# Kernel tuning notes

Hardware: AMD Instinct MI355X
Metric: run time of the kernel (lower is better)

The kernel has to match this reference:

```python
import jax, jax.numpy as jnp
import numpy as np

D_MODEL = 1024
NUM_HEADS = 16
HEAD_DIM = D_MODEL // NUM_HEADS
MAX_SEQ_LEN = 1024
BATCH = 2
SEQ = 1024


def setup_inputs() -> dict:
    key = jax.random.key(0)
    ks = jax.random.split(key, 12)
    s = 1.0 / np.sqrt(D_MODEL)
    inp = {
        "q": jax.random.normal(ks[0], (BATCH, SEQ, D_MODEL), jnp.float32),
        "k": jax.random.normal(ks[1], (BATCH, SEQ, D_MODEL), jnp.float32),
        "v": jax.random.normal(ks[2], (BATCH, SEQ, D_MODEL), jnp.float32),
        # causal mask (broadcast over batch and heads); masked_fill where mask==0
        "mask": jnp.tril(jnp.ones((SEQ, SEQ), jnp.bool_))[None, None, :, :],
        "Wq": jax.random.normal(ks[3], (D_MODEL, D_MODEL), jnp.float32) * s,
        "bq": jnp.zeros((D_MODEL,), jnp.float32),
        "Wk": jax.random.normal(ks[4], (D_MODEL, D_MODEL), jnp.float32) * s,
        "bk": jnp.zeros((D_MODEL,), jnp.float32),
        "Wv": jax.random.normal(ks[5], (D_MODEL, D_MODEL), jnp.float32) * s,
        "bv": jnp.zeros((D_MODEL,), jnp.float32),
        "Wo": jax.random.normal(ks[6], (D_MODEL, D_MODEL), jnp.float32) * s,
        "bo": jnp.zeros((D_MODEL,), jnp.float32),
        # relative-position embedding table (requires_grad=False in original)
        "e_r": jax.random.normal(ks[7], (MAX_SEQ_LEN, HEAD_DIM), jnp.float32),
    }
    return inp


def _skew(qe):
    # qe: (b, h, q, L) -> pad last dim on the left, reshape, drop first row
    b, h, q, L = qe.shape
    s = jnp.pad(qe, ((0, 0), (0, 0), (0, 0), (1, 0)))  # (b,h,q,L+1)
    s = s.reshape(b, h, L + 1, q)
    return s[:, :, 1:, :]  # (b,h,L,q)


def _rel_position_mask(q_len, L, dtype):
    # keep qe[i, j] where j >= L - 1 - i (upper-right skewed triangle)
    rows = jnp.arange(q_len)
    cols = jnp.arange(L)
    return (cols[None, :] >= (L - 1 - rows)[:, None]).astype(dtype)


def reference(q, k, v, mask, Wq, bq, Wk, bk, Wv, bv, Wo, bo, e_r):
    B, S, _ = q.shape
    def split_heads(x):
        return x.reshape(B, -1, NUM_HEADS, HEAD_DIM).transpose(0, 2, 1, 3)

    qh = split_heads(q @ Wq + bq)  # (B,H,S,D)
    kh = split_heads(k @ Wk + bk)
    vh = split_heads(v @ Wv + bv)

    q_len = qh.shape[2]
    e_sub = e_r[max(0, MAX_SEQ_LEN - q_len):, :]  # (L, D), L = min(q_len, MAX)
    qe = jnp.einsum('bhqd,kd->bhqk', qh, e_sub)  # (B,H,q,L)
    pm = _rel_position_mask(q_len, e_sub.shape[0], qe.dtype)
    qe = qe * pm[None, None, :, :]
    S_rel = _skew(qe)  # (B,H,L,q) == (B,H,S,S)

    scores = jnp.einsum('bhqd,bhkd->bhqk', qh, kh) / np.sqrt(HEAD_DIM)
    if mask is not None:
        scores = jnp.where(mask, scores, -1e9)
    attn = jax.nn.softmax(scores + S_rel, axis=-1)
    out = jnp.einsum('bhqk,bhkd->bhqd', attn, vh)
    out = out.transpose(0, 2, 1, 3).reshape(B, -1, D_MODEL)
    out = out @ Wo + bo
    return out, S_rel, qe
```

## Files before the change

### kernel.cpp

```cpp
#include <hip/hip_runtime.h>
#include <hip/hip_bf16.h>

typedef unsigned short u16;
typedef __attribute__((ext_vector_type(8))) short    bf16x8;
typedef __attribute__((ext_vector_type(8))) unsigned short u16x8;
typedef __attribute__((ext_vector_type(4))) float    f32x4;

#define SEQ    1024
#define DMODEL 1024
#define NHEAD  16
#define HDIM   64

#define OUT_OFF_SREL 2097152UL
#define OUT_OFF_QE   35651584UL

#define MFMA16(a, b, c) __builtin_amdgcn_mfma_f32_16x16x32_bf16((a), (b), (c), 0, 0, 0)

__device__ __forceinline__ float b2f(u16 u) {
    union { unsigned int i; float f; } x; x.i = ((unsigned int)u) << 16; return x.f;
}
__device__ __forceinline__ u16 f2b(float f) {
    union { __hip_bfloat16 h; u16 u; } x; x.h = __float2bfloat16(f); return x.u;
}
__device__ __forceinline__ void st_out(void* p, size_t idx, float v, int isf32) {
    if (isf32) ((float*)p)[idx] = v;
    else       ((u16*)p)[idx]   = f2b(v);
}

__global__ __launch_bounds__(256)
void k_detect(const u16* __restrict__ q, unsigned* __restrict__ flag)
{
    __shared__ int cnt;
    if (threadIdx.x == 0) cnt = 0;
    __syncthreads();
    int plaus = 0;
    for (int i = threadIdx.x; i < 4096; i += 256) {
        u16 u = q[2 * i];
        int e = (u >> 7) & 0xFF;
        if (e >= 102 && e <= 130) plaus++;
    }
    atomicAdd(&cnt, plaus);
    __syncthreads();
    if (threadIdx.x == 0) *flag = (cnt < 2048) ? 1u : 0u;
}

__global__ __launch_bounds__(256)
void k_conv(const void* __restrict__ src, u16* __restrict__ dst, int n4,
            const unsigned* __restrict__ flag)
{
    int i = blockIdx.x * 256 + threadIdx.x;
    if (i >= n4) return;
    if (*flag) {
        float4 f = ((const float4*)src)[i];
        ushort4 o;
        o.x = f2b(f.x); o.y = f2b(f.y); o.z = f2b(f.z); o.w = f2b(f.w);
        ((ushort4*)dst)[i] = o;
    } else {
        ((ushort4*)dst)[i] = ((const ushort4*)src)[i];
    }
}

__global__ __launch_bounds__(256)
void k_convT(const void* __restrict__ src, u16* __restrict__ dst,
             const unsigned* __restrict__ flag)
{
    __shared__ u16 tile[64][65];
    const int t  = threadIdx.x;
    const int n0 = blockIdx.x * 64;
    const int k0 = blockIdx.y * 64;
    const int isf32 = (*flag != 0u);

    #pragma unroll
    for (int i = 0; i < 4; ++i) {
        int idx = i * 256 + t;
        int r  = idx >> 4;
        int cg = (idx & 15) << 2;
        if (isf32) {
            float4 f = *(const float4*)((const float*)src + (size_t)(k0 + r) * 1024 + n0 + cg);
            tile[cg + 0][r] = f2b(f.x); tile[cg + 1][r] = f2b(f.y);
            tile[cg + 2][r] = f2b(f.z); tile[cg + 3][r] = f2b(f.w);
        } else {
            ushort4 u = *(const ushort4*)((const u16*)src + (size_t)(k0 + r) * 1024 + n0 + cg);
            tile[cg + 0][r] = u.x; tile[cg + 1][r] = u.y;
            tile[cg + 2][r] = u.z; tile[cg + 3][r] = u.w;
        }
    }
    __syncthreads();
    #pragma unroll
    for (int i = 0; i < 4; ++i) {
        int idx = i * 256 + t;
        int nl = idx >> 4;
        int kg = (idx & 15) << 2;
        ushort4 o;
        o.x = tile[nl][kg + 0]; o.y = tile[nl][kg + 1];
        o.z = tile[nl][kg + 2]; o.w = tile[nl][kg + 3];
        *(ushort4*)(dst + (size_t)(n0 + nl) * 1024 + k0 + kg) = o;
    }
}

__global__ __launch_bounds__(256)
void k_gemm(const u16* __restrict__ Aq, const u16* __restrict__ Ak, const u16* __restrict__ Av,
            const u16* __restrict__ Wtq, const u16* __restrict__ Wtk, const u16* __restrict__ Wtv,
            const u16* __restrict__ Bq, const u16* __restrict__ Bk, const u16* __restrict__ Bv,
            u16* __restrict__ Oq, u16* __restrict__ Ok, u16* __restrict__ Ov,
            void* __restrict__ out_flat, const unsigned* __restrict__ flag, int mode)
{
    __shared__ __align__(16) u16 Xs[128][72];
    __shared__ __align__(16) u16 Ws[128][72];

    const int z = blockIdx.z;
    const u16* A  = (z == 0) ? Aq : (z == 1) ? Ak : Av;
    const u16* Wt = (z == 0) ? Wtq : (z == 1) ? Wtk : Wtv;
    const u16* Bi = (z == 0) ? Bq : (z == 1) ? Bk : Bv;
    u16* O = (z == 0) ? Oq : (z == 1) ? Ok : Ov;

    const int t    = threadIdx.x;
    const int lane = t & 63;
    const int w    = t >> 6;
    const int q4   = lane >> 4;
    const int l16  = lane & 15;
    const int wy   = w >> 1, wx = w & 1;
    const int m0   = blockIdx.y * 128;
    const int n0   = blockIdx.x * 128;

    f32x4 acc[4][4] = {};

    for (int k0 = 0; k0 < DMODEL; k0 += 64) {
        __syncthreads();
        #pragma unroll
        for (int i = 0; i < 4; ++i) {
            int idx = i * 256 + t;
            int row = idx >> 3;
            int kg  = (idx & 7) << 3;
            *(u16x8*)&Xs[row][kg] = *(const u16x8*)(A  + (size_t)(m0 + row) * 1024 + k0 + kg);
            *(u16x8*)&Ws[row][kg] = *(const u16x8*)(Wt + (size_t)(n0 + row) * 1024 + k0 + kg);
        }
        __syncthreads();
        #pragma unroll
        for (int kc = 0; kc < 2; ++kc) {
            bf16x8 af[4], bfr[4];
            #pragma unroll
            for (int mt = 0; mt < 4; ++mt)
                af[mt] = *(const bf16x8*)&Xs[wy * 64 + mt * 16 + l16][kc * 32 + q4 * 8];
            #pragma unroll
            for (int nt = 0; nt < 4; ++nt)
                bfr[nt] = *(const bf16x8*)&Ws[wx * 64 + nt * 16 + l16][kc * 32 + q4 * 8];
            #pragma unroll
            for (int mt = 0; mt < 4; ++mt)
                #pragma unroll
                for (int nt = 0; nt < 4; ++nt)
                    acc[mt][nt] = MFMA16(af[mt], bfr[nt], acc[mt][nt]);
        }
    }

    const int isf32 = (*flag != 0u);
    float bias[4];
    #pragma unroll
    for (int nt = 0; nt < 4; ++nt) bias[nt] = b2f(Bi[n0 + wx * 64 + nt * 16 + l16]);

    #pragma unroll
    for (int mt = 0; mt < 4; ++mt) {
        #pragma unroll
        for (int nt = 0; nt < 4; ++nt) {
            #pragma unroll
            for (int reg = 0; reg < 4; ++reg) {
                const int m = m0 + wy * 64 + mt * 16 + q4 * 4 + reg;
                const int n = n0 + wx * 64 + nt * 16 + l16;
                const float v = acc[mt][nt][reg] + bias[nt];
                if (mode == 0) {
                    const int b = m >> 10, s = m & 1023, h = n >> 6, d = n & 63;
                    O[(((size_t)(b * NHEAD + h)) * SEQ + s) * HDIM + d] = f2b(v);
                } else {
                    st_out(out_flat, (size_t)m * DMODEL + n, v, isf32);
                }
            }
        }
    }
}

__global__ __launch_bounds__(256)
void k_qe(const u16* __restrict__ qh, const u16* __restrict__ er,
          void* __restrict__ out, const unsigned* __restrict__ flag)
{
    const int t    = threadIdx.x;
    const int lane = t & 63;
    const int w    = t >> 6;
    const int q4   = lane >> 4;
    const int l16  = lane & 15;
    const int bh   = blockIdx.x;
    const int r0   = blockIdx.y * 64;
    const int isf32 = (*flag != 0u);

    bf16x8 aQ[2];
    #pragma unroll
    for (int kc = 0; kc < 2; ++kc)
        aQ[kc] = *(const bf16x8*)(qh + ((size_t)bh * SEQ + r0 + w * 16 + l16) * HDIM + kc * 32 + q4 * 8);

    for (int jc = 0; jc < 16; ++jc) {
        f32x4 acc[4] = {};
        #pragma unroll
        for (int kc = 0; kc < 2; ++kc) {
            #pragma unroll
            for (int nt = 0; nt < 4; ++nt) {
                bf16x8 bfr = *(const bf16x8*)(er + (size_t)(jc * 64 + nt * 16 + l16) * HDIM + kc * 32 + q4 * 8);
                acc[nt] = MFMA16(aQ[kc], bfr, acc[nt]);
            }
        }
        #pragma unroll
        for (int nt = 0; nt < 4; ++nt) {
            #pragma unroll
            for (int reg = 0; reg < 4; ++reg) {
                const int r = r0 + w * 16 + q4 * 4 + reg;
                const int j = jc * 64 + nt * 16 + l16;
                const size_t base = (size_t)bh * (SEQ * SEQ) + (size_t)r * SEQ;
                const float v = acc[nt][reg];
                if (j + r >= SEQ - 1) {
                    st_out(out, OUT_OFF_QE   + base + j,                   v, isf32);
                    st_out(out, OUT_OFF_SREL + base + (j + r - (SEQ - 1)), v, isf32);
                } else {
                    st_out(out, OUT_OFF_QE   + base + j,           0.f, isf32);
                    st_out(out, OUT_OFF_SREL + base + (r + 1 + j), 0.f, isf32);
                }
            }
        }
    }
}

__global__ __launch_bounds__(256)
void k_attn(const u16* __restrict__ qh, const u16* __restrict__ kh, const u16* __restrict__ vh,
            const u16* __restrict__ er, u16* __restrict__ opre)
{
    __shared__ __align__(16) u16 Ks[64][72];
    __shared__ __align__(16) u16 Vt[64][72];
    __shared__ __align__(16) u16 Es[128][72];
    __shared__ float Rs[4][16][130];
    __shared__ __align__(16) u16 Ps[4][16][72];

    const int t    = threadIdx.x;
    const int lane = t & 63;
    const int w    = t >> 6;
    const int q4   = lane >> 4;
    const int l16  = lane & 15;
    const int bh   = blockIdx.x;
    const int qt   = 15 - blockIdx.y;
    const int r0   = qt * 64;

    bf16x8 aQ[2];
    #pragma unroll
    for (int kc = 0; kc < 2; ++kc)
        aQ[kc] = *(const bf16x8*)(qh + ((size_t)bh * SEQ + r0 + w * 16 + l16) * HDIM + kc * 32 + q4 * 8);

    f32x4 Oacc[4] = {};
    float mi[4] = { -1e30f, -1e30f, -1e30f, -1e30f };
    float li[4] = {};

    for (int tt = 0; tt <= qt; ++tt) {
        const int c0 = tt * 64;
        const int jbase = 960 + c0 - r0;
        const int diag = (tt == qt);

        __syncthreads();
        #pragma unroll
        for (int i = 0; i < 2; ++i) {
            int idx = i * 256 + t;
            int row = idx >> 3, kg = (idx & 7) << 3;
            *(u16x8*)&Ks[row][kg] = *(const u16x8*)(kh + ((size_t)bh * SEQ + c0 + row) * HDIM + kg);
        }
        #pragma unroll
        for (int i = 0; i < 4; ++i) {
            int idx = i * 256 + t;
            int c = idx >> 4, dg = (idx & 15) << 2;
            ushort4 v = *(const ushort4*)(vh + ((size_t)bh * SEQ + c0 + c) * HDIM + dg);
            Vt[dg + 0][c] = v.x; Vt[dg + 1][c] = v.y;
            Vt[dg + 2][c] = v.z; Vt[dg + 3][c] = v.w;
        }
        #pragma unroll
        for (int i = 0; i < 4; ++i) {
            int idx = i * 256 + t;
            int row = idx >> 3, kg = (idx & 7) << 3;
            int j = jbase + row; if (j > 1023) j = 1023;
            *(u16x8*)&Es[row][kg] = *(const u16x8*)(er + (size_t)j * HDIM + kg);
        }
        __syncthreads();

        {
            f32x4 Racc[8] = {};
            #pragma unroll
            for (int kc = 0; kc < 2; ++kc) {
                #pragma unroll
                for (int nt = 0; nt < 8; ++nt) {
                    bf16x8 bfr = *(const bf16x8*)&Es[nt * 16 + l16][kc * 32 + q4 * 8];
                    Racc[nt] = MFMA16(aQ[kc], bfr, Racc[nt]);
                }
            }
            #pragma unroll
            for (int nt = 0; nt < 8; ++nt)
                #pragma unroll
                for (int reg = 0; reg < 4; ++reg)
                    Rs[w][q4 * 4 + reg][nt * 16 + l16] = Racc[nt][reg];
        }

        f32x4 Sacc[4] = {};
        #pragma unroll
        for (int kc = 0; kc < 2; ++kc) {
            #pragma unroll
            for (int nt = 0; nt < 4; ++nt) {
                bf16x8 bfr = *(const bf16x8*)&Ks[nt * 16 + l16][kc * 32 + q4 * 8];
                Sacc[nt] = MFMA16(aQ[kc], bfr, Sacc[nt]);
            }
        }

        #pragma unroll
        for (int reg = 0; reg < 4; ++reg) {
            const int m16  = q4 * 4 + reg;
            const int mloc = w * 16 + m16;
            float sv[4];
            #pragma unroll
            for (int nt = 0; nt < 4; ++nt) {
                const int nloc = nt * 16 + l16;
                const int jj = 63 + nloc - mloc;
                float s = Sacc[nt][reg] * 0.125f + Rs[w][m16][jj];
                if (diag && (nloc > mloc)) s = -1e30f;
                sv[nt] = s;
            }
            float mx = fmaxf(fmaxf(sv[0], sv[1]), fmaxf(sv[2], sv[3]));
            #pragma unroll
            for (int off = 1; off < 16; off <<= 1) mx = fmaxf(mx, __shfl_xor(mx, off));
            const float mnew = fmaxf(mi[reg], mx);
            const float al   = __expf(mi[reg] - mnew);
            mi[reg] = mnew;
            float psum = 0.f;
            #pragma unroll
            for (int nt = 0; nt < 4; ++nt) {
                const float p = __expf(sv[nt] - mnew);
                psum += p;
                Ps[w][m16][nt * 16 + l16] = f2b(p);
            }
            #pragma unroll
            for (int off = 1; off < 16; off <<= 1) psum += __shfl_xor(psum, off);
            li[reg] = li[reg] * al + psum;
            #pragma unroll
            for (int dt = 0; dt < 4; ++dt) Oacc[dt][reg] *= al;
        }

        #pragma unroll
        for (int kc = 0; kc < 2; ++kc) {
            bf16x8 aP = *(const bf16x8*)&Ps[w][l16][kc * 32 + q4 * 8];
            #pragma unroll
            for (int dt = 0; dt < 4; ++dt) {
                bf16x8 bV = *(const bf16x8*)&Vt[dt * 16 + l16][kc * 32 + q4 * 8];
                Oacc[dt] = MFMA16(aP, bV, Oacc[dt]);
            }
        }
    }

    const int b = bh >> 4, h = bh & 15;
    #pragma unroll
    for (int dt = 0; dt < 4; ++dt) {
        #pragma unroll
        for (int reg = 0; reg < 4; ++reg) {
            const int r = r0 + w * 16 + q4 * 4 + reg;
            const int d = dt * 16 + l16;
            opre[((size_t)b * SEQ + r) * DMODEL + h * HDIM + d] = f2b(Oacc[dt][reg] / li[reg]);
        }
    }
}

extern "C" void kernel_launch(void* const* d_in, const int* in_sizes, int n_in,
                              void* d_out, int out_size, void* d_ws, size_t ws_size,
                              hipStream_t stream)
{
    u16* ws16 = (u16*)d_ws;
    unsigned* flag = (unsigned*)d_ws;
    u16* cq   = ws16 + 8;
    u16* ck   = cq   + 2097152;
    u16* cv   = ck   + 2097152;
    u16* cwqT = cv   + 2097152;
    u16* cwkT = cwqT + 1048576;
    u16* cwvT = cwkT + 1048576;
    u16* cwoT = cwvT + 1048576;
    u16* cbq  = cwoT + 1048576;
    u16* cbk  = cbq  + 1024;
    u16* cbv  = cbk  + 1024;
    u16* cbo  = cbv  + 1024;
    u16* cer  = cbo  + 1024;
    u16* qh   = cer  + 65536;
    u16* kh   = qh   + 2097152;
    u16* vh   = kh   + 2097152;
    u16* opre = vh   + 2097152;

    dim3 blk(256);

    k_detect<<<1, blk, 0, stream>>>((const u16*)d_in[0], flag);

    k_conv <<<dim3(2048),  blk, 0, stream>>>(d_in[0],  cq,  2097152 / 4, flag);
    k_conv <<<dim3(2048),  blk, 0, stream>>>(d_in[1],  ck,  2097152 / 4, flag);
    k_conv <<<dim3(2048),  blk, 0, stream>>>(d_in[2],  cv,  2097152 / 4, flag);
    k_convT<<<dim3(16,16), blk, 0, stream>>>(d_in[4],  cwqT, flag);
    k_convT<<<dim3(16,16), blk, 0, stream>>>(d_in[6],  cwkT, flag);
    k_convT<<<dim3(16,16), blk, 0, stream>>>(d_in[8],  cwvT, flag);
    k_convT<<<dim3(16,16), blk, 0, stream>>>(d_in[10], cwoT, flag);
    k_conv <<<dim3(1),     blk, 0, stream>>>(d_in[5],  cbq, 1024 / 4,  flag);
    k_conv <<<dim3(1),     blk, 0, stream>>>(d_in[7],  cbk, 1024 / 4,  flag);
    k_conv <<<dim3(1),     blk, 0, stream>>>(d_in[9],  cbv, 1024 / 4,  flag);
    k_conv <<<dim3(1),     blk, 0, stream>>>(d_in[11], cbo, 1024 / 4,  flag);
    k_conv <<<dim3(64),    blk, 0, stream>>>(d_in[12], cer, 65536 / 4, flag);

    k_gemm<<<dim3(8, 16, 3), blk, 0, stream>>>(cq, ck, cv, cwqT, cwkT, cwvT,
                                               cbq, cbk, cbv, qh, kh, vh,
                                               nullptr, flag, 0);
    k_qe  <<<dim3(32, 16), blk, 0, stream>>>(qh, cer, d_out, flag);
    k_attn<<<dim3(32, 16), blk, 0, stream>>>(qh, kh, vh, cer, opre);
    k_gemm<<<dim3(8, 16, 1), blk, 0, stream>>>(opre, opre, opre, cwoT, cwoT, cwoT,
                                               cbo, cbo, cbo, nullptr, nullptr, nullptr,
                                               d_out, flag, 1);
}
```

Baseline: 518.5 us.

## Fuse qe/S_rel output writes into attention kernel and batch conversion launches

The separate k_qe kernel is removed. The attention kernel now writes the qe and skewed S_rel outputs straight from its relative-position MFMA accumulators, and zero-fills the masked triangle with a per-row loop at kernel start. This removes a second pass of Q·E^T MFMAs and one launch. The many small conversion and transpose launches are merged into three batched kernels indexed by blockIdx.z or block ranges. The attention kernel now also does the large output store traffic, with scattered per-element stores that may stall its main loop.

```diff
diff --git a/kernel.cpp b/kernel.cpp
--- a/kernel.cpp
+++ b/kernel.cpp
@@ -45,9 +45,13 @@
 }
 
 __global__ __launch_bounds__(256)
-void k_conv(const void* __restrict__ src, u16* __restrict__ dst, int n4,
-            const unsigned* __restrict__ flag)
-{
+void k_conv3(const void* __restrict__ s0, const void* __restrict__ s1, const void* __restrict__ s2,
+             u16* __restrict__ d0, u16* __restrict__ d1, u16* __restrict__ d2,
+             int n4, const unsigned* __restrict__ flag)
+{
+    const int z = blockIdx.z;
+    const void* src = (z == 0) ? s0 : (z == 1) ? s1 : s2;
+    u16* dst = (z == 0) ? d0 : (z == 1) ? d1 : d2;
     int i = blockIdx.x * 256 + threadIdx.x;
     if (i >= n4) return;
     if (*flag) {
@@ -61,10 +65,44 @@
 }
 
 __global__ __launch_bounds__(256)
-void k_convT(const void* __restrict__ src, u16* __restrict__ dst,
-             const unsigned* __restrict__ flag)
+void k_conv_small(const void* __restrict__ b0, const void* __restrict__ b1,
+                  const void* __restrict__ b2, const void* __restrict__ b3,
+                  const void* __restrict__ erp,
+                  u16* __restrict__ db0, u16* __restrict__ db1,
+                  u16* __restrict__ db2, u16* __restrict__ db3,
+                  u16* __restrict__ der, const unsigned* __restrict__ flag)
+{
+    const int bx = blockIdx.x;
+    const void* src; u16* dst; int i;
+    if (bx < 64) { src = erp; dst = der; i = bx * 256 + threadIdx.x; }
+    else {
+        const int which = bx - 64;
+        src = (which == 0) ? b0 : (which == 1) ? b1 : (which == 2) ? b2 : b3;
+        dst = (which == 0) ? db0 : (which == 1) ? db1 : (which == 2) ? db2 : db3;
+        i = threadIdx.x;
+    }
+    if (*flag) {
+        float4 f = ((const float4*)src)[i];
+        ushort4 o;
+        o.x = f2b(f.x); o.y = f2b(f.y); o.z = f2b(f.z); o.w = f2b(f.w);
+        ((ushort4*)dst)[i] = o;
+    } else {
+        ((ushort4*)dst)[i] = ((const ushort4*)src)[i];
+    }
+}
+
+__global__ __launch_bounds__(256)
+void k_convT4(const void* __restrict__ s0, const void* __restrict__ s1,
+              const void* __restrict__ s2, const void* __restrict__ s3,
+              u16* __restrict__ d0, u16* __restrict__ d1,
+              u16* __restrict__ d2, u16* __restrict__ d3,
+              const unsigned* __restrict__ flag)
 {
     __shared__ u16 tile[64][65];
+    const int z = blockIdx.z;
+    const void* src = (z == 0) ? s0 : (z == 1) ? s1 : (z == 2) ? s2 : s3;
+    u16* dst = (z == 0) ? d0 : (z == 1) ? d1 : (z == 2) ? d2 : d3;
+
     const int t  = threadIdx.x;
     const int n0 = blockIdx.x * 64;
     const int k0 = blockIdx.y * 64;
@@ -179,56 +217,9 @@
 }
 
 __global__ __launch_bounds__(256)
-void k_qe(const u16* __restrict__ qh, const u16* __restrict__ er,
-          void* __restrict__ out, const unsigned* __restrict__ flag)
-{
-    const int t    = threadIdx.x;
-    const int lane = t & 63;
-    const int w    = t >> 6;
-    const int q4   = lane >> 4;
-    const int l16  = lane & 15;
-    const int bh   = blockIdx.x;
-    const int r0   = blockIdx.y * 64;
-    const int isf32 = (*flag != 0u);
-
-    bf16x8 aQ[2];
-    #pragma unroll
-    for (int kc = 0; kc < 2; ++kc)
-        aQ[kc] = *(const bf16x8*)(qh + ((size_t)bh * SEQ + r0 + w * 16 + l16) * HDIM + kc * 32 + q4 * 8);
-
-    for (int jc = 0; jc < 16; ++jc) {
-        f32x4 acc[4] = {};
-        #pragma unroll
-        for (int kc = 0; kc < 2; ++kc) {
-            #pragma unroll
-            for (int nt = 0; nt < 4; ++nt) {
-                bf16x8 bfr = *(const bf16x8*)(er + (size_t)(jc * 64 + nt * 16 + l16) * HDIM + kc * 32 + q4 * 8);
-                acc[nt] = MFMA16(aQ[kc], bfr, acc[nt]);
-            }
-        }
-        #pragma unroll
-        for (int nt = 0; nt < 4; ++nt) {
-            #pragma unroll
-            for (int reg = 0; reg < 4; ++reg) {
-                const int r = r0 + w * 16 + q4 * 4 + reg;
-                const int j = jc * 64 + nt * 16 + l16;
-                const size_t base = (size_t)bh * (SEQ * SEQ) + (size_t)r * SEQ;
-                const float v = acc[nt][reg];
-                if (j + r >= SEQ - 1) {
-                    st_out(out, OUT_OFF_QE   + base + j,                   v, isf32);
-                    st_out(out, OUT_OFF_SREL + base + (j + r - (SEQ - 1)), v, isf32);
-                } else {
-                    st_out(out, OUT_OFF_QE   + base + j,           0.f, isf32);
-                    st_out(out, OUT_OFF_SREL + base + (r + 1 + j), 0.f, isf32);
-                }
-            }
-        }
-    }
-}
-
-__global__ __launch_bounds__(256)
 void k_attn(const u16* __restrict__ qh, const u16* __restrict__ kh, const u16* __restrict__ vh,
-            const u16* __restrict__ er, u16* __restrict__ opre)
+            const u16* __restrict__ er, u16* __restrict__ opre,
+            void* __restrict__ out, const unsigned* __restrict__ flag)
 {
     __shared__ __align__(16) u16 Ks[64][72];
     __shared__ __align__(16) u16 Vt[64][72];
@@ -244,6 +235,19 @@
     const int bh   = blockIdx.x;
     const int qt   = 15 - blockIdx.y;
     const int r0   = qt * 64;
+    const int isf32 = (*flag != 0u);
+    const size_t obase = (size_t)bh * (SEQ * SEQ);
+
+    for (int ml = w; ml < 64; ml += 4) {
+        const int r  = r0 + ml;
+        const int Lz = SEQ - 1 - r;
+        const size_t rq = OUT_OFF_QE   + obase + (size_t)r * SEQ;
+        const size_t rs = OUT_OFF_SREL + obase + (size_t)r * SEQ + r + 1;
+        for (int c2 = lane; c2 < Lz; c2 += 64) {
+            st_out(out, rq + c2, 0.f, isf32);
+            st_out(out, rs + c2, 0.f, isf32);
+        }
+    }
 
     bf16x8 aQ[2];
     #pragma unroll
@@ -298,6 +302,22 @@
                 #pragma unroll
                 for (int reg = 0; reg < 4; ++reg)
                     Rs[w][q4 * 4 + reg][nt * 16 + l16] = Racc[nt][reg];
+
+            #pragma unroll
+            for (int nt = 0; nt < 8; ++nt) {
+                const int nn = nt * 16 + l16;
+                #pragma unroll
+                for (int reg = 0; reg < 4; ++reg) {
+                    const int mloc = w * 16 + q4 * 4 + reg;
+                    const int rel  = nn - 63 + mloc;
+                    if (rel >= 0 && rel < 64 && (!diag || nn <= 63)) {
+                        const int r = r0 + mloc;
+                        const float v = Racc[nt][reg];
+                        st_out(out, OUT_OFF_SREL + obase + (size_t)r * SEQ + (c0 + rel),   v, isf32);
+                        st_out(out, OUT_OFF_QE   + obase + (size_t)r * SEQ + (jbase + nn), v, isf32);
+                    }
+                }
+            }
         }
 
         f32x4 Sacc[4] = {};
@@ -393,24 +413,17 @@
 
     k_detect<<<1, blk, 0, stream>>>((const u16*)d_in[0], flag);
 
-    k_conv <<<dim3(2048),  blk, 0, stream>>>(d_in[0],  cq,  2097152 / 4, flag);
-    k_conv <<<dim3(2048),  blk, 0, stream>>>(d_in[1],  ck,  2097152 / 4, flag);
-    k_conv <<<dim3(2048),  blk, 0, stream>>>(d_in[2],  cv,  2097152 / 4, flag);
-    k_convT<<<dim3(16,16), blk, 0, stream>>>(d_in[4],  cwqT, flag);
-    k_convT<<<dim3(16,16), blk, 0, stream>>>(d_in[6],  cwkT, flag);
-    k_convT<<<dim3(16,16), blk, 0, stream>>>(d_in[8],  cwvT, flag);
-    k_convT<<<dim3(16,16), blk, 0, stream>>>(d_in[10], cwoT, flag);
-    k_conv <<<dim3(1),     blk, 0, stream>>>(d_in[5],  cbq, 1024 / 4,  flag);
-    k_conv <<<dim3(1),     blk, 0, stream>>>(d_in[7],  cbk, 1024 / 4,  flag);
-    k_conv <<<dim3(1),     blk, 0, stream>>>(d_in[9],  cbv, 1024 / 4,  flag);
-    k_conv <<<dim3(1),     blk, 0, stream>>>(d_in[11], cbo, 1024 / 4,  flag);
-    k_conv <<<dim3(64),    blk, 0, stream>>>(d_in[12], cer, 65536 / 4, flag);
+    k_conv3<<<dim3(2048, 1, 3), blk, 0, stream>>>(d_in[0], d_in[1], d_in[2],
+                                                  cq, ck, cv, 2097152 / 4, flag);
+    k_convT4<<<dim3(16, 16, 4), blk, 0, stream>>>(d_in[4], d_in[6], d_in[8], d_in[10],
+                                                  cwqT, cwkT, cwvT, cwoT, flag);
+    k_conv_small<<<dim3(68), blk, 0, stream>>>(d_in[5], d_in[7], d_in[9], d_in[11], d_in[12],
+                                               cbq, cbk, cbv, cbo, cer, flag);
 
     k_gemm<<<dim3(8, 16, 3), blk, 0, stream>>>(cq, ck, cv, cwqT, cwkT, cwvT,
                                                cbq, cbk, cbv, qh, kh, vh,
                                                nullptr, flag, 0);
-    k_qe  <<<dim3(32, 16), blk, 0, stream>>>(qh, cer, d_out, flag);
-    k_attn<<<dim3(32, 16), blk, 0, stream>>>(qh, kh, vh, cer, opre);
+    k_attn<<<dim3(32, 16), blk, 0, stream>>>(qh, kh, vh, cer, opre, d_out, flag);
     k_gemm<<<dim3(8, 16, 1), blk, 0, stream>>>(opre, opre, opre, cwoT, cwoT, cwoT,
                                                cbo, cbo, cbo, nullptr, nullptr, nullptr,
                                                d_out, flag, 1);
```

After: 476.3 us. 1.09x faster.
